# Kernel optimization log

Hardware: AMD Instinct MI355X
Metric: run time of the kernel (lower is better)

## Reference

```python
import jax, jax.numpy as jnp
import numpy as np

B, C_IN, T = 256, 1024, 128   # batch, encoder channels, spectrogram frames (2**15 samples / 256 hop)
CTX, N_EVENTS = 64, 16        # context_dim, n_events (module constants)


def setup_inputs() -> dict:
    key = jax.random.key(0)
    k0, k1, k2 = jax.random.split(key, 3)
    return {
        "encoded": jax.random.normal(k0, (B, C_IN, T), dtype=jnp.float32),
        "w_vec": jax.random.normal(k1, (CTX, C_IN), dtype=jnp.float32) * 0.02,
        "b_vec": jnp.zeros((CTX,), dtype=jnp.float32),
        "w_switch": jax.random.normal(k2, (1, C_IN), dtype=jnp.float32) * 0.02,
        "b_switch": jnp.zeros((1,), dtype=jnp.float32),
    }


def reference(encoded, w_vec, b_vec, w_switch, b_switch):
    # 1x1 Conv1d == per-timestep matmul
    event_vecs = jnp.einsum('bct,dc->btd', encoded, w_vec) + b_vec          # [B,T,CTX]
    switch = jnp.einsum('bct,c->bt', encoded, w_switch[0]) + b_switch[0]    # [B,T]
    attn = jax.nn.relu(switch)                                              # [B,T]

    # sparsify: keep top-k attention values and their indices
    vals, idx = jax.lax.top_k(attn, N_EVENTS)                               # [B,K]

    # sparsify_vectors: gather event vectors at top-k time indices
    vecs = jnp.take_along_axis(event_vecs, idx[:, :, None], axis=1)         # [B,K,CTX]

    # scheduling[b, j, idx[b,j]] = attn[b, idx[b,j]] (vectorized scatter,
    # replaces the original nested python-loop scalar scatter)
    b_idx = jnp.arange(B)[:, None]
    j_idx = jnp.arange(N_EVENTS)[None, :]
    scheduling = jnp.zeros((B, N_EVENTS, T), dtype=attn.dtype)
    scheduling = scheduling.at[b_idx, j_idx, idx].set(vals)                 # [B,K,T]

    return vecs, scheduling
```

## Files before the change

kernel.cpp:

```cpp
#include <hip/hip_runtime.h>
#include <hip/hip_bf16.h>

#define C_IN 1024
#define T_SZ 128
#define CTX 64
#define NEV 16
#define BK 64
#define NTILE 16
#define NTHR 512
#define BROW 72
#define PLROW 132

#define BF_OFF 0
#define WB_OFF 36864
#define WS_OFF 55296
#define SP_OFF 59392
#define AT_OFF 63488
#define TV_OFF 64000
#define TI_OFF 64064
#define ARENA_SZ 64128

typedef short bf16x8 __attribute__((ext_vector_type(8)));
typedef float f32x4 __attribute__((ext_vector_type(4)));

__device__ __forceinline__ unsigned short f2bf(float f) {
  __hip_bfloat16 h = __float2bfloat16(f);
  return *(unsigned short*)&h;
}

#define BARRIER() do { \
  asm volatile("s_waitcnt lgkmcnt(0)" ::: "memory"); \
  __builtin_amdgcn_s_barrier(); \
} while (0)

#define ISSUE(kt, ev, wv) do { \
  const float* _s = encB + (kt) * (BK * T_SZ) + cb0 * T_SZ + t0; \
  _Pragma("unroll") for (int _j = 0; _j < 8; ++_j) \
    ev[_j] = *(const float2*)(_s + _j * T_SZ); \
  const float* _w = wvec + wd * C_IN + (kt) * BK + wc; \
  wv[0] = *(const float4*)_w; \
  wv[1] = *(const float4*)(_w + 4); \
} while (0)

#define CONVERT(kt, ev, wv, buf) do { \
  const float* _wt = wswl + (kt) * BK + cb0; \
  union { bf16x8 v; unsigned short u[8]; } _p0, _p1, _pw; \
  _Pragma("unroll") for (int _j = 0; _j < 8; ++_j) { \
    sw0 = fmaf(ev[_j].x, _wt[_j], sw0); \
    sw1 = fmaf(ev[_j].y, _wt[_j], sw1); \
    _p0.u[_j] = f2bf(ev[_j].x); \
    _p1.u[_j] = f2bf(ev[_j].y); \
  } \
  *(bf16x8*)&Bf[((buf) * T_SZ + t0) * BROW + cb0] = _p0.v; \
  *(bf16x8*)&Bf[((buf) * T_SZ + t0 + 1) * BROW + cb0] = _p1.v; \
  _pw.u[0] = f2bf(wv[0].x); _pw.u[1] = f2bf(wv[0].y); \
  _pw.u[2] = f2bf(wv[0].z); _pw.u[3] = f2bf(wv[0].w); \
  _pw.u[4] = f2bf(wv[1].x); _pw.u[5] = f2bf(wv[1].y); \
  _pw.u[6] = f2bf(wv[1].z); _pw.u[7] = f2bf(wv[1].w); \
  *(bf16x8*)&Wb[((buf) * CTX + wd) * BROW + wc] = _pw.v; \
} while (0)

#define MFMA_TILE(buf) do { \
  _Pragma("unroll") for (int _ks = 0; _ks < 2; ++_ks) { \
    bf16x8 _bv = *(const bf16x8*)&Bf[((buf) * T_SZ + n0 + tl) * BROW + _ks * 32 + g * 8]; \
    bf16x8 _a0 = *(const bf16x8*)&Wb[((buf) * CTX +  0 + tl) * BROW + _ks * 32 + g * 8]; \
    bf16x8 _a1 = *(const bf16x8*)&Wb[((buf) * CTX + 16 + tl) * BROW + _ks * 32 + g * 8]; \
    bf16x8 _a2 = *(const bf16x8*)&Wb[((buf) * CTX + 32 + tl) * BROW + _ks * 32 + g * 8]; \
    bf16x8 _a3 = *(const bf16x8*)&Wb[((buf) * CTX + 48 + tl) * BROW + _ks * 32 + g * 8]; \
    acc0 = __builtin_amdgcn_mfma_f32_16x16x32_bf16(_a0, _bv, acc0, 0, 0, 0); \
    acc1 = __builtin_amdgcn_mfma_f32_16x16x32_bf16(_a1, _bv, acc1, 0, 0, 0); \
    acc2 = __builtin_amdgcn_mfma_f32_16x16x32_bf16(_a2, _bv, acc2, 0, 0, 0); \
    acc3 = __builtin_amdgcn_mfma_f32_16x16x32_bf16(_a3, _bv, acc3, 0, 0, 0); \
  } \
} while (0)

__global__ __launch_bounds__(NTHR, 1) void fused_sparsify(
    const float* __restrict__ enc,
    const float* __restrict__ wvec,
    const float* __restrict__ bvec,
    const float* __restrict__ wsw,
    const float* __restrict__ bsw,
    float* __restrict__ out)
{
  const int b    = blockIdx.x;
  const int tid  = threadIdx.x;
  const int lane = tid & 63;
  const int wid  = tid >> 6;
  const int g    = lane >> 4;
  const int tl   = lane & 15;
  const int n0   = wid * 16;

  const int cb0 = wid * 8;
  const int t0  = 2 * lane;
  const int wd  = tid >> 3;
  const int wc  = (tid & 7) * 8;

  __shared__ __align__(16) char arena[ARENA_SZ];
  unsigned short* Bf = (unsigned short*)(arena + BF_OFF);
  unsigned short* Wb = (unsigned short*)(arena + WB_OFF);
  float* wswl = (float*)(arena + WS_OFF);
  float* swp  = (float*)(arena + SP_OFF);
  float* attn = (float*)(arena + AT_OFF);
  float* topv = (float*)(arena + TV_OFF);
  int*   topi = (int*)(arena + TI_OFF);

  const float* encB = enc + (size_t)b * (C_IN * T_SZ);

  wswl[tid]       = wsw[tid];
  wswl[tid + 512] = wsw[tid + 512];

  f32x4 acc0 = {0.f, 0.f, 0.f, 0.f};
  f32x4 acc1 = acc0, acc2 = acc0, acc3 = acc0;
  float sw0 = 0.f, sw1 = 0.f;

  float2 evA[8], evB[8];
  float4 wvA[2], wvB[2];

  ISSUE(0, evA, wvA);
  ISSUE(1, evB, wvB);
  BARRIER();
  CONVERT(0, evA, wvA, 0);
  BARRIER();

#pragma unroll 1
  for (int t = 0; t < NTILE; t += 2) {
    if (t + 2 < NTILE) ISSUE(t + 2, evA, wvA);
    MFMA_TILE(0);
    CONVERT(t + 1, evB, wvB, 1);
    BARRIER();
    if (t + 3 < NTILE) ISSUE(t + 3, evB, wvB);
    MFMA_TILE(1);
    if (t + 2 < NTILE) CONVERT(t + 2, evA, wvA, 0);
    BARRIER();
  }

  float* Pl = (float*)(arena + BF_OFF);
#pragma unroll
  for (int r = 0; r < 4; ++r) {
    Pl[( 0 + 4 * g + r) * PLROW + n0 + tl] = acc0[r];
    Pl[(16 + 4 * g + r) * PLROW + n0 + tl] = acc1[r];
    Pl[(32 + 4 * g + r) * PLROW + n0 + tl] = acc2[r];
    Pl[(48 + 4 * g + r) * PLROW + n0 + tl] = acc3[r];
  }
  swp[wid * T_SZ + t0]     = sw0;
  swp[wid * T_SZ + t0 + 1] = sw1;
  __syncthreads();

  if (tid < T_SZ) {
    float s = 0.f;
#pragma unroll
    for (int k = 0; k < 8; ++k) s += swp[k * T_SZ + tid];
    attn[tid] = fmaxf(s + bsw[0], 0.f);
  }
  __syncthreads();

  if (tid < 64) {
    float v0 = attn[tid], v1 = attn[tid + 64];
#pragma unroll 1
    for (int r = 0; r < NEV; ++r) {
      float bv; int bi;
      if (v0 >= v1) { bv = v0; bi = tid; } else { bv = v1; bi = tid + 64; }
#pragma unroll
      for (int off = 32; off > 0; off >>= 1) {
        float ov = __shfl_xor(bv, off, 64);
        int   oi = __shfl_xor(bi, off, 64);
        if (ov > bv || (ov == bv && oi < bi)) { bv = ov; bi = oi; }
      }
      if (bi == tid) v0 = -__builtin_inff();
      if (bi == tid + 64) v1 = -__builtin_inff();
      if (tid == r) { topv[r] = bv; topi[r] = bi; }
    }
  }
  __syncthreads();

  {
    float* os = out + (256 * NEV * CTX) + b * (NEV * T_SZ);
    int j  = tid >> 5;
    int tt = (tid * 4) & 127;
    float tv = topv[j];
    int   ti = topi[j];
    float4 v;
    v.x = (tt + 0 == ti) ? tv : 0.f;
    v.y = (tt + 1 == ti) ? tv : 0.f;
    v.z = (tt + 2 == ti) ? tv : 0.f;
    v.w = (tt + 3 == ti) ? tv : 0.f;
    *(float4*)&os[tid * 4] = v;
  }
  {
    float* ov = out + b * (NEV * CTX);
#pragma unroll
    for (int s = 0; s < 2; ++s) {
      int o = s * NTHR + tid;
      int j = o >> 6, d = o & 63;
      ov[o] = Pl[d * PLROW + topi[j]] + bvec[d];
    }
  }
}

extern "C" void kernel_launch(void* const* d_in, const int* in_sizes, int n_in,
                              void* d_out, int out_size, void* d_ws, size_t ws_size,
                              hipStream_t stream) {
  const float* enc  = (const float*)d_in[0];
  const float* wvec = (const float*)d_in[1];
  const float* bvec = (const float*)d_in[2];
  const float* wsw  = (const float*)d_in[3];
  const float* bsw  = (const float*)d_in[4];
  float* o = (float*)d_out;
  (void)in_sizes; (void)n_in; (void)out_size; (void)d_ws; (void)ws_size;
  fused_sparsify<<<256, NTHR, 0, stream>>>(enc, wvec, bvec, wsw, bsw, o);
}
```

Baseline: 35.86 us.

## Preload bf16 weights into LDS fragments and feed encoder directly from registers

Instead of staging both encoder tiles and weight tiles through LDS each K-step, the kernel converts the whole 64x1024 weight matrix to bf16 once into LDS, laid out in MFMA fragment order. Each wave then loads its own encoder columns straight from global memory into registers as the B operand, with triple buffering. This removes the per-tile barriers and the LDS round trip for activations, and the switch reduction is done with shuffles instead of a shared-memory pass. In exchange it uses about 133KB of LDS and more registers, and the global loads are strided scalar loads rather than vectorised ones.

```diff
diff --git a/kernel.cpp b/kernel.cpp
--- a/kernel.cpp
+++ b/kernel.cpp
@@ -5,20 +5,15 @@
 #define T_SZ 128
 #define CTX 64
 #define NEV 16
-#define BK 64
 #define NTILE 16
 #define NTHR 512
-#define BROW 72
 #define PLROW 132
 
-#define BF_OFF 0
-#define WB_OFF 36864
-#define WS_OFF 55296
-#define SP_OFF 59392
-#define AT_OFF 63488
-#define TV_OFF 64000
-#define TI_OFF 64064
-#define ARENA_SZ 64128
+#define WS_OFF 131072
+#define AT_OFF 135168
+#define TV_OFF 135680
+#define TI_OFF 135744
+#define ARENA_SZ 135808
 
 typedef short bf16x8 __attribute__((ext_vector_type(8)));
 typedef float f32x4 __attribute__((ext_vector_type(4)));
@@ -33,46 +28,34 @@
   __builtin_amdgcn_s_barrier(); \
 } while (0)
 
-#define ISSUE(kt, ev, wv) do { \
-  const float* _s = encB + (kt) * (BK * T_SZ) + cb0 * T_SZ + t0; \
-  _Pragma("unroll") for (int _j = 0; _j < 8; ++_j) \
-    ev[_j] = *(const float2*)(_s + _j * T_SZ); \
-  const float* _w = wvec + wd * C_IN + (kt) * BK + wc; \
-  wv[0] = *(const float4*)_w; \
-  wv[1] = *(const float4*)(_w + 4); \
-} while (0)
+#define ISSUE(kt, ev) do { \
+  _Pragma("unroll") for (int _ks = 0; _ks < 2; ++_ks) { \
+    const float* _bp = encB + ((kt) * 64 + _ks * 32 + g8) * T_SZ + ncol; \
+    _Pragma("unroll") for (int _j = 0; _j < 8; ++_j) \
+      ev[_ks * 8 + _j] = _bp[_j * T_SZ]; \
+  } } while (0)
 
-#define CONVERT(kt, ev, wv, buf) do { \
-  const float* _wt = wswl + (kt) * BK + cb0; \
-  union { bf16x8 v; unsigned short u[8]; } _p0, _p1, _pw; \
-  _Pragma("unroll") for (int _j = 0; _j < 8; ++_j) { \
-    sw0 = fmaf(ev[_j].x, _wt[_j], sw0); \
-    sw1 = fmaf(ev[_j].y, _wt[_j], sw1); \
-    _p0.u[_j] = f2bf(ev[_j].x); \
-    _p1.u[_j] = f2bf(ev[_j].y); \
-  } \
-  *(bf16x8*)&Bf[((buf) * T_SZ + t0) * BROW + cb0] = _p0.v; \
-  *(bf16x8*)&Bf[((buf) * T_SZ + t0 + 1) * BROW + cb0] = _p1.v; \
-  _pw.u[0] = f2bf(wv[0].x); _pw.u[1] = f2bf(wv[0].y); \
-  _pw.u[2] = f2bf(wv[0].z); _pw.u[3] = f2bf(wv[0].w); \
-  _pw.u[4] = f2bf(wv[1].x); _pw.u[5] = f2bf(wv[1].y); \
-  _pw.u[6] = f2bf(wv[1].z); _pw.u[7] = f2bf(wv[1].w); \
-  *(bf16x8*)&Wb[((buf) * CTX + wd) * BROW + wc] = _pw.v; \
-} while (0)
-
-#define MFMA_TILE(buf) do { \
+#define COMPUTE(kt, ev) do { \
   _Pragma("unroll") for (int _ks = 0; _ks < 2; ++_ks) { \
-    bf16x8 _bv = *(const bf16x8*)&Bf[((buf) * T_SZ + n0 + tl) * BROW + _ks * 32 + g * 8]; \
-    bf16x8 _a0 = *(const bf16x8*)&Wb[((buf) * CTX +  0 + tl) * BROW + _ks * 32 + g * 8]; \
-    bf16x8 _a1 = *(const bf16x8*)&Wb[((buf) * CTX + 16 + tl) * BROW + _ks * 32 + g * 8]; \
-    bf16x8 _a2 = *(const bf16x8*)&Wb[((buf) * CTX + 32 + tl) * BROW + _ks * 32 + g * 8]; \
-    bf16x8 _a3 = *(const bf16x8*)&Wb[((buf) * CTX + 48 + tl) * BROW + _ks * 32 + g * 8]; \
-    acc0 = __builtin_amdgcn_mfma_f32_16x16x32_bf16(_a0, _bv, acc0, 0, 0, 0); \
-    acc1 = __builtin_amdgcn_mfma_f32_16x16x32_bf16(_a1, _bv, acc1, 0, 0, 0); \
-    acc2 = __builtin_amdgcn_mfma_f32_16x16x32_bf16(_a2, _bv, acc2, 0, 0, 0); \
-    acc3 = __builtin_amdgcn_mfma_f32_16x16x32_bf16(_a3, _bv, acc3, 0, 0, 0); \
-  } \
-} while (0)
+    const f32x4* _wp = (const f32x4*)(wswl + (kt) * 64 + _ks * 32 + g8); \
+    f32x4 _w0 = _wp[0], _w1 = _wp[1]; \
+    union { bf16x8 v; unsigned short u[8]; } _bu; \
+    _Pragma("unroll") for (int _j = 0; _j < 4; ++_j) { \
+      sw = fmaf(ev[_ks * 8 + _j], _w0[_j], sw); \
+      sw = fmaf(ev[_ks * 8 + 4 + _j], _w1[_j], sw); \
+      _bu.u[_j]     = f2bf(ev[_ks * 8 + _j]); \
+      _bu.u[4 + _j] = f2bf(ev[_ks * 8 + 4 + _j]); \
+    } \
+    const char* _fb = arena + (((kt) * 2 + _ks) * 4) * 1024 + lane * 16; \
+    bf16x8 _a0 = *(const bf16x8*)(_fb); \
+    bf16x8 _a1 = *(const bf16x8*)(_fb + 1024); \
+    bf16x8 _a2 = *(const bf16x8*)(_fb + 2048); \
+    bf16x8 _a3 = *(const bf16x8*)(_fb + 3072); \
+    acc0 = __builtin_amdgcn_mfma_f32_16x16x32_bf16(_a0, _bu.v, acc0, 0, 0, 0); \
+    acc1 = __builtin_amdgcn_mfma_f32_16x16x32_bf16(_a1, _bu.v, acc1, 0, 0, 0); \
+    acc2 = __builtin_amdgcn_mfma_f32_16x16x32_bf16(_a2, _bu.v, acc2, 0, 0, 0); \
+    acc3 = __builtin_amdgcn_mfma_f32_16x16x32_bf16(_a3, _bu.v, acc3, 0, 0, 0); \
+  } } while (0)
 
 __global__ __launch_bounds__(NTHR, 1) void fused_sparsify(
     const float* __restrict__ enc,
@@ -87,72 +70,72 @@
   const int lane = tid & 63;
   const int wid  = tid >> 6;
   const int g    = lane >> 4;
+  const int g8   = g * 8;
   const int tl   = lane & 15;
   const int n0   = wid * 16;
-
-  const int cb0 = wid * 8;
-  const int t0  = 2 * lane;
-  const int wd  = tid >> 3;
-  const int wc  = (tid & 7) * 8;
+  const int ncol = n0 + tl;
 
   __shared__ __align__(16) char arena[ARENA_SZ];
-  unsigned short* Bf = (unsigned short*)(arena + BF_OFF);
-  unsigned short* Wb = (unsigned short*)(arena + WB_OFF);
   float* wswl = (float*)(arena + WS_OFF);
-  float* swp  = (float*)(arena + SP_OFF);
   float* attn = (float*)(arena + AT_OFF);
   float* topv = (float*)(arena + TV_OFF);
   int*   topi = (int*)(arena + TI_OFF);
 
   const float* encB = enc + (size_t)b * (C_IN * T_SZ);
+  const float bsw0 = bsw[0];
 
+  f32x4 acc0 = {0.f, 0.f, 0.f, 0.f};
+  f32x4 acc1 = acc0, acc2 = acc0, acc3 = acc0;
+  float sw = 0.f;
+
+  float evA[16], evB[16], evC[16];
+
+  ISSUE(0, evA);
+
+#pragma unroll 4
+  for (int i = 0; i < 16; ++i) {
+    const int f   = wid * 16 + i;
+    const int kt  = f >> 3;
+    const int ks  = (f >> 2) & 1;
+    const int acc = f & 3;
+    const float* wp = wvec + (acc * 16 + tl) * C_IN + kt * 64 + ks * 32 + g8;
+    float4 w0 = *(const float4*)wp;
+    float4 w1 = *(const float4*)(wp + 4);
+    union { bf16x8 v; unsigned short u[8]; } pk;
+    pk.u[0] = f2bf(w0.x); pk.u[1] = f2bf(w0.y); pk.u[2] = f2bf(w0.z); pk.u[3] = f2bf(w0.w);
+    pk.u[4] = f2bf(w1.x); pk.u[5] = f2bf(w1.y); pk.u[6] = f2bf(w1.z); pk.u[7] = f2bf(w1.w);
+    *(bf16x8*)(arena + f * 1024 + lane * 16) = pk.v;
+  }
   wswl[tid]       = wsw[tid];
   wswl[tid + 512] = wsw[tid + 512];
 
-  f32x4 acc0 = {0.f, 0.f, 0.f, 0.f};
-  f32x4 acc1 = acc0, acc2 = acc0, acc3 = acc0;
-  float sw0 = 0.f, sw1 = 0.f;
-
-  float2 evA[8], evB[8];
-  float4 wvA[2], wvB[2];
-
-  ISSUE(0, evA, wvA);
-  ISSUE(1, evB, wvB);
-  BARRIER();
-  CONVERT(0, evA, wvA, 0);
+  ISSUE(1, evB);
   BARRIER();
 
 #pragma unroll 1
-  for (int t = 0; t < NTILE; t += 2) {
-    if (t + 2 < NTILE) ISSUE(t + 2, evA, wvA);
-    MFMA_TILE(0);
-    CONVERT(t + 1, evB, wvB, 1);
-    BARRIER();
-    if (t + 3 < NTILE) ISSUE(t + 3, evB, wvB);
-    MFMA_TILE(1);
-    if (t + 2 < NTILE) CONVERT(t + 2, evA, wvA, 0);
-    BARRIER();
+  for (int t0 = 0; t0 < 15; t0 += 3) {
+    ISSUE(t0 + 2, evC);
+    COMPUTE(t0, evA);
+    if (t0 + 3 < NTILE) ISSUE(t0 + 3, evA);
+    COMPUTE(t0 + 1, evB);
+    if (t0 + 4 < NTILE) ISSUE(t0 + 4, evB);
+    COMPUTE(t0 + 2, evC);
   }
+  COMPUTE(15, evA);
 
-  float* Pl = (float*)(arena + BF_OFF);
+  sw += __shfl_xor(sw, 16, 64);
+  sw += __shfl_xor(sw, 32, 64);
+  if (lane < 16) attn[ncol] = fmaxf(sw + bsw0, 0.f);
+  __syncthreads();
+
+  float* Pl = (float*)arena;
 #pragma unroll
   for (int r = 0; r < 4; ++r) {
-    Pl[( 0 + 4 * g + r) * PLROW + n0 + tl] = acc0[r];
-    Pl[(16 + 4 * g + r) * PLROW + n0 + tl] = acc1[r];
-    Pl[(32 + 4 * g + r) * PLROW + n0 + tl] = acc2[r];
-    Pl[(48 + 4 * g + r) * PLROW + n0 + tl] = acc3[r];
+    Pl[( 0 + 4 * g + r) * PLROW + ncol] = acc0[r];
+    Pl[(16 + 4 * g + r) * PLROW + ncol] = acc1[r];
+    Pl[(32 + 4 * g + r) * PLROW + ncol] = acc2[r];
+    Pl[(48 + 4 * g + r) * PLROW + ncol] = acc3[r];
   }
-  swp[wid * T_SZ + t0]     = sw0;
-  swp[wid * T_SZ + t0 + 1] = sw1;
-  __syncthreads();
-
-  if (tid < T_SZ) {
-    float s = 0.f;
-#pragma unroll
-    for (int k = 0; k < 8; ++k) s += swp[k * T_SZ + tid];
-    attn[tid] = fmaxf(s + bsw[0], 0.f);
-  }
-  __syncthreads();
 
   if (tid < 64) {
     float v0 = attn[tid], v1 = attn[tid + 64];
```

Measured after the change: 41.61 us. +16.0%, slower.

## Split channel reduction across two blocks per batch with a combine kernel

Applied to the files above, without the earlier changes.

Splits the 1024-channel reduction into two halves, so 512 blocks each process 512 channels per batch, doubling the grid to fill more CUs. Each partial block writes its full 64x128 event-vector partial (as bf16) and its switch partial sums to workspace. A second kernel sums the halves, applies relu, runs top-k, and gathers and scatters the outputs. This adds a second launch and workspace round-trips, and the partials are rounded to bf16 before they are added.

```diff
diff --git a/kernel.cpp b/kernel.cpp
--- a/kernel.cpp
+++ b/kernel.cpp
@@ -6,7 +6,7 @@
 #define CTX 64
 #define NEV 16
 #define BK 64
-#define NTILE 16
+#define NTILE 8
 #define NTHR 512
 #define BROW 72
 #define PLROW 132
@@ -14,11 +14,10 @@
 #define BF_OFF 0
 #define WB_OFF 36864
 #define WS_OFF 55296
-#define SP_OFF 59392
-#define AT_OFF 63488
-#define TV_OFF 64000
-#define TI_OFF 64064
-#define ARENA_SZ 64128
+#define SP_OFF 57344
+#define ARENA_SZ 61440
+
+#define WSP_BYTES (512 * 8192 * 2)
 
 typedef short bf16x8 __attribute__((ext_vector_type(8)));
 typedef float f32x4 __attribute__((ext_vector_type(4)));
@@ -26,6 +25,11 @@
 __device__ __forceinline__ unsigned short f2bf(float f) {
   __hip_bfloat16 h = __float2bfloat16(f);
   return *(unsigned short*)&h;
+}
+__device__ __forceinline__ float bf2f(unsigned short u) {
+  union { unsigned int i; float f; } x;
+  x.i = ((unsigned int)u) << 16;
+  return x.f;
 }
 
 #define BARRIER() do { \
@@ -37,7 +41,7 @@
   const float* _s = encB + (kt) * (BK * T_SZ) + cb0 * T_SZ + t0; \
   _Pragma("unroll") for (int _j = 0; _j < 8; ++_j) \
     ev[_j] = *(const float2*)(_s + _j * T_SZ); \
-  const float* _w = wvec + wd * C_IN + (kt) * BK + wc; \
+  const float* _w = wvec + wd * C_IN + hoff + (kt) * BK + wc; \
   wv[0] = *(const float4*)_w; \
   wv[1] = *(const float4*)(_w + 4); \
 } while (0)
@@ -71,18 +75,17 @@
     acc1 = __builtin_amdgcn_mfma_f32_16x16x32_bf16(_a1, _bv, acc1, 0, 0, 0); \
     acc2 = __builtin_amdgcn_mfma_f32_16x16x32_bf16(_a2, _bv, acc2, 0, 0, 0); \
     acc3 = __builtin_amdgcn_mfma_f32_16x16x32_bf16(_a3, _bv, acc3, 0, 0, 0); \
-  } \
-} while (0)
-
-__global__ __launch_bounds__(NTHR, 1) void fused_sparsify(
+  } } while (0)
+
+__global__ __launch_bounds__(NTHR, 4) void part_kernel(
     const float* __restrict__ enc,
     const float* __restrict__ wvec,
-    const float* __restrict__ bvec,
     const float* __restrict__ wsw,
-    const float* __restrict__ bsw,
-    float* __restrict__ out)
+    unsigned short* __restrict__ wsP,
+    float* __restrict__ wsS)
 {
-  const int b    = blockIdx.x;
+  const int h    = blockIdx.x >> 8;
+  const int b    = blockIdx.x & 255;
   const int tid  = threadIdx.x;
   const int lane = tid & 63;
   const int wid  = tid >> 6;
@@ -94,20 +97,17 @@
   const int t0  = 2 * lane;
   const int wd  = tid >> 3;
   const int wc  = (tid & 7) * 8;
+  const int hoff = h * 512;
 
   __shared__ __align__(16) char arena[ARENA_SZ];
   unsigned short* Bf = (unsigned short*)(arena + BF_OFF);
   unsigned short* Wb = (unsigned short*)(arena + WB_OFF);
   float* wswl = (float*)(arena + WS_OFF);
   float* swp  = (float*)(arena + SP_OFF);
-  float* attn = (float*)(arena + AT_OFF);
-  float* topv = (float*)(arena + TV_OFF);
-  int*   topi = (int*)(arena + TI_OFF);
-
-  const float* encB = enc + (size_t)b * (C_IN * T_SZ);
-
-  wswl[tid]       = wsw[tid];
-  wswl[tid + 512] = wsw[tid + 512];
+
+  const float* encB = enc + (size_t)b * (C_IN * T_SZ) + (size_t)hoff * T_SZ;
+
+  wswl[tid] = wsw[hoff + tid];
 
   f32x4 acc0 = {0.f, 0.f, 0.f, 0.f};
   f32x4 acc1 = acc0, acc2 = acc0, acc3 = acc0;
@@ -150,8 +150,35 @@
     float s = 0.f;
 #pragma unroll
     for (int k = 0; k < 8; ++k) s += swp[k * T_SZ + tid];
-    attn[tid] = fmaxf(s + bsw[0], 0.f);
-  }
+    wsS[(h * 256 + b) * T_SZ + tid] = s;
+  }
+  {
+    const int d = tid >> 3, tc = (tid & 7) * 16;
+    const float* pr = Pl + d * PLROW + tc;
+    union { uint4 q[2]; unsigned short u[16]; } pk;
+#pragma unroll
+    for (int i = 0; i < 16; ++i) pk.u[i] = f2bf(pr[i]);
+    uint4* dst = (uint4*)(wsP + (size_t)(h * 256 + b) * 8192 + tid * 16);
+    dst[0] = pk.q[0];
+    dst[1] = pk.q[1];
+  }
+}
+
+__global__ __launch_bounds__(128) void combine_kernel(
+    const unsigned short* __restrict__ wsP,
+    const float* __restrict__ wsS,
+    const float* __restrict__ bvec,
+    const float* __restrict__ bsw,
+    float* __restrict__ out)
+{
+  const int b   = blockIdx.x;
+  const int tid = threadIdx.x;
+
+  __shared__ float attn[T_SZ];
+  __shared__ float topv[NEV];
+  __shared__ int   topi[NEV];
+
+  attn[tid] = fmaxf(wsS[b * T_SZ + tid] + wsS[(256 + b) * T_SZ + tid] + bsw[0], 0.f);
   __syncthreads();
 
   if (tid < 64) {
@@ -175,24 +202,31 @@
 
   {
     float* os = out + (256 * NEV * CTX) + b * (NEV * T_SZ);
-    int j  = tid >> 5;
-    int tt = (tid * 4) & 127;
-    float tv = topv[j];
-    int   ti = topi[j];
-    float4 v;
-    v.x = (tt + 0 == ti) ? tv : 0.f;
-    v.y = (tt + 1 == ti) ? tv : 0.f;
-    v.z = (tt + 2 == ti) ? tv : 0.f;
-    v.w = (tt + 3 == ti) ? tv : 0.f;
-    *(float4*)&os[tid * 4] = v;
-  }
+    const int j  = tid >> 3;
+    const int tt = (tid & 7) * 16;
+    const float tv = topv[j];
+    const int   ti = topi[j];
+#pragma unroll
+    for (int q = 0; q < 4; ++q) {
+      float4 v;
+      v.x = (tt + q * 4 + 0 == ti) ? tv : 0.f;
+      v.y = (tt + q * 4 + 1 == ti) ? tv : 0.f;
+      v.z = (tt + q * 4 + 2 == ti) ? tv : 0.f;
+      v.w = (tt + q * 4 + 3 == ti) ? tv : 0.f;
+      *(float4*)&os[tid * 16 + q * 4] = v;
+    }
+  }
+
   {
     float* ov = out + b * (NEV * CTX);
-#pragma unroll
-    for (int s = 0; s < 2; ++s) {
-      int o = s * NTHR + tid;
+    const unsigned short* p0 = wsP + (size_t)b * 8192;
+    const unsigned short* p1 = wsP + (size_t)(256 + b) * 8192;
+#pragma unroll
+    for (int i = 0; i < 8; ++i) {
+      int o = i * 128 + tid;
       int j = o >> 6, d = o & 63;
-      ov[o] = Pl[d * PLROW + topi[j]] + bvec[d];
+      int ti = topi[j];
+      ov[o] = bf2f(p0[d * T_SZ + ti]) + bf2f(p1[d * T_SZ + ti]) + bvec[d];
     }
   }
 }
@@ -206,6 +240,9 @@
   const float* wsw  = (const float*)d_in[3];
   const float* bsw  = (const float*)d_in[4];
   float* o = (float*)d_out;
-  (void)in_sizes; (void)n_in; (void)out_size; (void)d_ws; (void)ws_size;
-  fused_sparsify<<<256, NTHR, 0, stream>>>(enc, wvec, bvec, wsw, bsw, o);
-}
+  unsigned short* wsP = (unsigned short*)d_ws;
+  float* wsS = (float*)((char*)d_ws + WSP_BYTES);
+  (void)in_sizes; (void)n_in; (void)out_size; (void)ws_size;
+  part_kernel<<<512, NTHR, 0, stream>>>(enc, wvec, wsw, wsP, wsS);
+  combine_kernel<<<256, 128, 0, stream>>>(wsP, wsS, bvec, bsw, o);
+}
```

After: 41.20 us. 1.15x slower.

## Give each wave private time columns and drop per-tile block barriers

Applied to the files above, without the earlier changes.

Restructures the GEMM so each wave loads and converts only its own 16 time columns of the encoder tile into a wave-private LDS buffer. It no longer shares a cooperatively staged tile, so the two block-wide barriers per K-tile go away. Weight fragments are now loaded straight from global into registers in MFMA layout and converted there, which removes the shared weight LDS buffer. The switch reduction becomes a wave shuffle reduction instead of a partial-sum LDS pass. In exchange, every wave re-reads the full weight matrix from global/L2 each tile, register pressure is higher (16 float4 per thread), and the loop is fully unrolled.

```diff
diff --git a/kernel.cpp b/kernel.cpp
--- a/kernel.cpp
+++ b/kernel.cpp
@@ -5,20 +5,17 @@
 #define T_SZ 128
 #define CTX 64
 #define NEV 16
-#define BK 64
 #define NTILE 16
 #define NTHR 512
 #define BROW 72
 #define PLROW 132
 
 #define BF_OFF 0
-#define WB_OFF 36864
-#define WS_OFF 55296
-#define SP_OFF 59392
-#define AT_OFF 63488
-#define TV_OFF 64000
-#define TI_OFF 64064
-#define ARENA_SZ 64128
+#define WS_OFF 36864
+#define AT_OFF 40960
+#define TV_OFF 41472
+#define TI_OFF 41536
+#define ARENA_SZ 41600
 
 typedef short bf16x8 __attribute__((ext_vector_type(8)));
 typedef float f32x4 __attribute__((ext_vector_type(4)));
@@ -28,50 +25,55 @@
   return *(unsigned short*)&h;
 }
 
-#define BARRIER() do { \
-  asm volatile("s_waitcnt lgkmcnt(0)" ::: "memory"); \
-  __builtin_amdgcn_s_barrier(); \
-} while (0)
-
-#define ISSUE(kt, ev, wv) do { \
-  const float* _s = encB + (kt) * (BK * T_SZ) + cb0 * T_SZ + t0; \
+#define ISSUE_E(kt, ev) do { \
+  const float* _s = encB + ((kt) * 64 + cg * 8) * T_SZ + n0 + 2 * tp; \
   _Pragma("unroll") for (int _j = 0; _j < 8; ++_j) \
     ev[_j] = *(const float2*)(_s + _j * T_SZ); \
-  const float* _w = wvec + wd * C_IN + (kt) * BK + wc; \
-  wv[0] = *(const float4*)_w; \
-  wv[1] = *(const float4*)(_w + 4); \
-} while (0)
-
-#define CONVERT(kt, ev, wv, buf) do { \
-  const float* _wt = wswl + (kt) * BK + cb0; \
-  union { bf16x8 v; unsigned short u[8]; } _p0, _p1, _pw; \
+} while (0)
+
+#define ISSUE_W(kt) do { \
+  _Pragma("unroll") for (int _a = 0; _a < 4; ++_a) \
+  _Pragma("unroll") for (int _k = 0; _k < 2; ++_k) { \
+    const float* _w = wvec + (_a * 16 + tl) * C_IN + (kt) * 64 + _k * 32 + g * 8; \
+    wW[(_a * 2 + _k) * 2 + 0] = *(const float4*)_w; \
+    wW[(_a * 2 + _k) * 2 + 1] = *(const float4*)(_w + 4); \
+  } } while (0)
+
+#define CVTWRITE(kt, ev, buf) do { \
+  const float* _wt = wswl + (kt) * 64 + cg * 8; \
+  union { bf16x8 v; unsigned short u[8]; } _p0, _p1; \
   _Pragma("unroll") for (int _j = 0; _j < 8; ++_j) { \
     sw0 = fmaf(ev[_j].x, _wt[_j], sw0); \
     sw1 = fmaf(ev[_j].y, _wt[_j], sw1); \
     _p0.u[_j] = f2bf(ev[_j].x); \
     _p1.u[_j] = f2bf(ev[_j].y); \
   } \
-  *(bf16x8*)&Bf[((buf) * T_SZ + t0) * BROW + cb0] = _p0.v; \
-  *(bf16x8*)&Bf[((buf) * T_SZ + t0 + 1) * BROW + cb0] = _p1.v; \
-  _pw.u[0] = f2bf(wv[0].x); _pw.u[1] = f2bf(wv[0].y); \
-  _pw.u[2] = f2bf(wv[0].z); _pw.u[3] = f2bf(wv[0].w); \
-  _pw.u[4] = f2bf(wv[1].x); _pw.u[5] = f2bf(wv[1].y); \
-  _pw.u[6] = f2bf(wv[1].z); _pw.u[7] = f2bf(wv[1].w); \
-  *(bf16x8*)&Wb[((buf) * CTX + wd) * BROW + wc] = _pw.v; \
-} while (0)
-
-#define MFMA_TILE(buf) do { \
-  _Pragma("unroll") for (int _ks = 0; _ks < 2; ++_ks) { \
-    bf16x8 _bv = *(const bf16x8*)&Bf[((buf) * T_SZ + n0 + tl) * BROW + _ks * 32 + g * 8]; \
-    bf16x8 _a0 = *(const bf16x8*)&Wb[((buf) * CTX +  0 + tl) * BROW + _ks * 32 + g * 8]; \
-    bf16x8 _a1 = *(const bf16x8*)&Wb[((buf) * CTX + 16 + tl) * BROW + _ks * 32 + g * 8]; \
-    bf16x8 _a2 = *(const bf16x8*)&Wb[((buf) * CTX + 32 + tl) * BROW + _ks * 32 + g * 8]; \
-    bf16x8 _a3 = *(const bf16x8*)&Wb[((buf) * CTX + 48 + tl) * BROW + _ks * 32 + g * 8]; \
-    acc0 = __builtin_amdgcn_mfma_f32_16x16x32_bf16(_a0, _bv, acc0, 0, 0, 0); \
-    acc1 = __builtin_amdgcn_mfma_f32_16x16x32_bf16(_a1, _bv, acc1, 0, 0, 0); \
-    acc2 = __builtin_amdgcn_mfma_f32_16x16x32_bf16(_a2, _bv, acc2, 0, 0, 0); \
-    acc3 = __builtin_amdgcn_mfma_f32_16x16x32_bf16(_a3, _bv, acc3, 0, 0, 0); \
-  } \
+  *(bf16x8*)&BfW[((buf) * 16 + 2 * tp    ) * BROW + cg * 8] = _p0.v; \
+  *(bf16x8*)&BfW[((buf) * 16 + 2 * tp + 1) * BROW + cg * 8] = _p1.v; \
+} while (0)
+
+#define MF1(_k, AIDX, ACC, BV) do { \
+  union { bf16x8 v; unsigned short u[8]; } _pa; \
+  float4 _w0 = wW[(AIDX * 2 + _k) * 2], _w1 = wW[(AIDX * 2 + _k) * 2 + 1]; \
+  _pa.u[0] = f2bf(_w0.x); _pa.u[1] = f2bf(_w0.y); _pa.u[2] = f2bf(_w0.z); _pa.u[3] = f2bf(_w0.w); \
+  _pa.u[4] = f2bf(_w1.x); _pa.u[5] = f2bf(_w1.y); _pa.u[6] = f2bf(_w1.z); _pa.u[7] = f2bf(_w1.w); \
+  ACC = __builtin_amdgcn_mfma_f32_16x16x32_bf16(_pa.v, BV, ACC, 0, 0, 0); \
+} while (0)
+
+#define COMPUTE(buf) do { \
+  _Pragma("unroll") for (int _k = 0; _k < 2; ++_k) { \
+    bf16x8 _bv = *(const bf16x8*)&BfW[((buf) * 16 + tl) * BROW + _k * 32 + g * 8]; \
+    MF1(_k, 0, acc0, _bv); \
+    MF1(_k, 1, acc1, _bv); \
+    MF1(_k, 2, acc2, _bv); \
+    MF1(_k, 3, acc3, _bv); \
+  } } while (0)
+
+#define STEP(T, SA, SB) do { \
+  ISSUE_W(T); \
+  if ((T) + 2 < NTILE) ISSUE_E((T) + 2, ev##SA); \
+  if ((T) + 1 < NTILE) CVTWRITE((T) + 1, ev##SB, ((T) + 1) & 1); \
+  COMPUTE((T) & 1); \
 } while (0)
 
 __global__ __launch_bounds__(NTHR, 1) void fused_sparsify(
@@ -89,50 +91,47 @@
   const int g    = lane >> 4;
   const int tl   = lane & 15;
   const int n0   = wid * 16;
-
-  const int cb0 = wid * 8;
-  const int t0  = 2 * lane;
-  const int wd  = tid >> 3;
-  const int wc  = (tid & 7) * 8;
+  const int cg   = lane >> 3;
+  const int tp   = lane & 7;
 
   __shared__ __align__(16) char arena[ARENA_SZ];
-  unsigned short* Bf = (unsigned short*)(arena + BF_OFF);
-  unsigned short* Wb = (unsigned short*)(arena + WB_OFF);
+  unsigned short* Bf   = (unsigned short*)(arena + BF_OFF);
+  unsigned short* BfW  = Bf + wid * (2 * 16 * BROW);
   float* wswl = (float*)(arena + WS_OFF);
-  float* swp  = (float*)(arena + SP_OFF);
   float* attn = (float*)(arena + AT_OFF);
   float* topv = (float*)(arena + TV_OFF);
   int*   topi = (int*)(arena + TI_OFF);
 
   const float* encB = enc + (size_t)b * (C_IN * T_SZ);
-
-  wswl[tid]       = wsw[tid];
-  wswl[tid + 512] = wsw[tid + 512];
+  const float bsw0 = bsw[0];
 
   f32x4 acc0 = {0.f, 0.f, 0.f, 0.f};
   f32x4 acc1 = acc0, acc2 = acc0, acc3 = acc0;
   float sw0 = 0.f, sw1 = 0.f;
 
   float2 evA[8], evB[8];
-  float4 wvA[2], wvB[2];
-
-  ISSUE(0, evA, wvA);
-  ISSUE(1, evB, wvB);
-  BARRIER();
-  CONVERT(0, evA, wvA, 0);
-  BARRIER();
-
-#pragma unroll 1
-  for (int t = 0; t < NTILE; t += 2) {
-    if (t + 2 < NTILE) ISSUE(t + 2, evA, wvA);
-    MFMA_TILE(0);
-    CONVERT(t + 1, evB, wvB, 1);
-    BARRIER();
-    if (t + 3 < NTILE) ISSUE(t + 3, evB, wvB);
-    MFMA_TILE(1);
-    if (t + 2 < NTILE) CONVERT(t + 2, evA, wvA, 0);
-    BARRIER();
-  }
+  float4 wW[16];
+
+  ISSUE_E(0, evA);
+  ISSUE_E(1, evB);
+  wswl[tid]       = wsw[tid];
+  wswl[tid + 512] = wsw[tid + 512];
+  __syncthreads();
+  CVTWRITE(0, evA, 0);
+
+  STEP( 0, A, B); STEP( 1, B, A); STEP( 2, A, B); STEP( 3, B, A);
+  STEP( 4, A, B); STEP( 5, B, A); STEP( 6, A, B); STEP( 7, B, A);
+  STEP( 8, A, B); STEP( 9, B, A); STEP(10, A, B); STEP(11, B, A);
+  STEP(12, A, B); STEP(13, B, A); STEP(14, A, B); STEP(15, B, A);
+
+  sw0 += __shfl_xor(sw0, 8, 64);  sw1 += __shfl_xor(sw1, 8, 64);
+  sw0 += __shfl_xor(sw0, 16, 64); sw1 += __shfl_xor(sw1, 16, 64);
+  sw0 += __shfl_xor(sw0, 32, 64); sw1 += __shfl_xor(sw1, 32, 64);
+  if (cg == 0) {
+    attn[n0 + 2 * tp]     = fmaxf(sw0 + bsw0, 0.f);
+    attn[n0 + 2 * tp + 1] = fmaxf(sw1 + bsw0, 0.f);
+  }
+  __syncthreads();
 
   float* Pl = (float*)(arena + BF_OFF);
 #pragma unroll
@@ -141,16 +140,6 @@
     Pl[(16 + 4 * g + r) * PLROW + n0 + tl] = acc1[r];
     Pl[(32 + 4 * g + r) * PLROW + n0 + tl] = acc2[r];
     Pl[(48 + 4 * g + r) * PLROW + n0 + tl] = acc3[r];
-  }
-  swp[wid * T_SZ + t0]     = sw0;
-  swp[wid * T_SZ + t0 + 1] = sw1;
-  __syncthreads();
-
-  if (tid < T_SZ) {
-    float s = 0.f;
-#pragma unroll
-    for (int k = 0; k < 8; ++k) s += swp[k * T_SZ + tid];
-    attn[tid] = fmaxf(s + bsw[0], 0.f);
   }
   __syncthreads();
 
```

New measurement: 79.55 us. 122% more time.
